# Kernel optimization log

Hardware: AMD Instinct MI355X
Metric: run time of the kernel (lower is better)

The kernel has to match this reference:

```python
import jax, jax.numpy as jnp
import numpy as np

D = 1024      # atrybuty (d_model)
H = 16        # kanaly (heads)
DH = D // H   # head dim
B, T = 4, 2048
EPS = 1e-5


def setup_inputs() -> dict:
    key = jax.random.key(0)
    ks = jax.random.split(key, 16)
    s = 0.02
    return {
        "x":  jax.random.normal(ks[0], (B, T, D), jnp.float32),
        "wq": jax.random.normal(ks[1], (D, D), jnp.float32) * s,
        "wk": jax.random.normal(ks[2], (D, D), jnp.float32) * s,
        "wv": jax.random.normal(ks[3], (D, D), jnp.float32) * s,
        "wp": jax.random.normal(ks[4], (D, D), jnp.float32) * s,
        "bp": jnp.zeros((D,), jnp.float32),
        "w1": jax.random.normal(ks[5], (D, 4 * D), jnp.float32) * s,
        "b1": jnp.zeros((4 * D,), jnp.float32),
        "w2": jax.random.normal(ks[6], (4 * D, D), jnp.float32) * s,
        "b2": jnp.zeros((D,), jnp.float32),
        "g1": jnp.ones((D,), jnp.float32),
        "be1": jnp.zeros((D,), jnp.float32),
        "g2": jnp.ones((D,), jnp.float32),
        "be2": jnp.zeros((D,), jnp.float32),
    }


def _layernorm(x, g, b):
    mu = jnp.mean(x, axis=-1, keepdims=True)
    var = jnp.mean(jnp.square(x - mu), axis=-1, keepdims=True)
    return (x - mu) * jax.lax.rsqrt(var + EPS) * g + b


def reference(x, wq, wk, wv, wp, bp, w1, b1, w2, b2, g1, be1, g2, be2):
    b, t, d = x.shape
    # --- self-attention on ln1(x) ---
    h = _layernorm(x, g1, be1)
    # per-head Linears are equivalent to one [D,D] projection split into heads
    q = (h @ wq).reshape(b, t, H, DH).transpose(0, 2, 1, 3)  # [B,H,T,Dh]
    k = (h @ wk).reshape(b, t, H, DH).transpose(0, 2, 1, 3)
    v = (h @ wv).reshape(b, t, H, DH).transpose(0, 2, 1, 3)
    # NOTE: original scales by full embed dim C, not head_dim
    scale = jnp.asarray(d, x.dtype) ** -0.5
    wei = jnp.einsum("bhqd,bhkd->bhqk", q, k) * scale
    causal = jnp.tril(jnp.ones((t, t), bool))
    wei = jnp.where(causal, wei, -jnp.inf)
    wei = jax.nn.softmax(wei, axis=-1)
    att = jnp.einsum("bhqk,bhkd->bhqd", wei, v)
    att = att.transpose(0, 2, 1, 3).reshape(b, t, d)
    x = x + att @ wp + bp
    # --- feedforward on ln2(x) ---
    h2 = _layernorm(x, g2, be2)
    x = x + jax.nn.relu(h2 @ w1 + b1) @ w2 + b2
    return x
```

## Files before the change

kernel.cpp:

```cpp
#include <hip/hip_runtime.h>
#include <hip/hip_bf16.h>
#include <stdint.h>

#define DM   1024
#define NH   16
#define DH   64
#define BATCH 4
#define SEQ  2048
#define MROWS (BATCH*SEQ)

typedef float f32x4 __attribute__((ext_vector_type(4)));
typedef __bf16 bf16x8 __attribute__((ext_vector_type(8)));
typedef short s16x4 __attribute__((ext_vector_type(4)));
typedef int   i32x2 __attribute__((ext_vector_type(2)));

#define QSCALE 0.045084220f

#define VM(n) asm volatile("s_waitcnt vmcnt(" #n ")" ::: "memory")
#define LGKM0 do { asm volatile("s_waitcnt lgkmcnt(0)" ::: "memory"); \
                   __builtin_amdgcn_sched_barrier(0); } while (0)

__device__ __forceinline__ short f2bs(float f) {
    __bf16 h = (__bf16)f;
    return __builtin_bit_cast(short, h);
}

__device__ __forceinline__ void gload_lds16(const void* g, void* l) {
    __builtin_amdgcn_global_load_lds(
        (__attribute__((address_space(1))) void*)(g),
        (__attribute__((address_space(3))) void*)(l), 16, 0, 0);
}

__device__ __forceinline__ void swz_xy(int ny, int& x, int& y) {
    const int bid = blockIdx.x;
    const int cpx = gridDim.x >> 3;
    const int wg  = (bid & 7) * cpx + (bid >> 3);
    x = wg / ny;
    y = wg % ny;
}

__global__ __launch_bounds__(256) void transpose_cvt_kernel(
    const float* __restrict__ w, short* __restrict__ wt, int K, int N)
{
    __shared__ short tile[64 * 65];
    const int k0 = blockIdx.x * 64, n0 = blockIdx.y * 64;
    const int t = threadIdx.x;
#pragma unroll
    for (int i = 0; i < 16; ++i) {
        int idx = i * 256 + t;
        int r = idx >> 6, c = idx & 63;
        tile[r * 65 + c] = f2bs(w[(size_t)(k0 + r) * N + n0 + c]);
    }
    __syncthreads();
#pragma unroll
    for (int i = 0; i < 16; ++i) {
        int idx = i * 256 + t;
        int r = idx >> 6, c = idx & 63;
        wt[(size_t)(n0 + r) * K + k0 + c] = tile[c * 65 + r];
    }
}

__global__ __launch_bounds__(256) void ln_kernel(
    const float* __restrict__ x, const float* __restrict__ g,
    const float* __restrict__ be, short* __restrict__ out)
{
    const int row = blockIdx.x, t = threadIdx.x;
    const float4 v = ((const float4*)(x + (size_t)row * DM))[t];
    float s  = v.x + v.y + v.z + v.w;
    float ss = v.x * v.x + v.y * v.y + v.z * v.z + v.w * v.w;
#pragma unroll
    for (int d = 1; d < 64; d <<= 1) {
        s  += __shfl_xor(s, d, 64);
        ss += __shfl_xor(ss, d, 64);
    }
    __shared__ float red[8];
    const int wid = t >> 6;
    if ((t & 63) == 0) { red[wid] = s; red[wid + 4] = ss; }
    __syncthreads();
    s  = red[0] + red[1] + red[2] + red[3];
    ss = red[4] + red[5] + red[6] + red[7];
    const float mu = s * (1.0f / DM);
    const float rs = rsqrtf(ss * (1.0f / DM) - mu * mu + 1e-5f);
    const float4 gg = ((const float4*)g)[t];
    const float4 bb = ((const float4*)be)[t];
    short4 o;
    o.x = f2bs((v.x - mu) * rs * gg.x + bb.x);
    o.y = f2bs((v.y - mu) * rs * gg.y + bb.y);
    o.z = f2bs((v.z - mu) * rs * gg.z + bb.z);
    o.w = f2bs((v.w - mu) * rs * gg.w + bb.w);
    ((short4*)(out + (size_t)row * DM))[t] = o;
}

template<int NCHUNK>
__device__ __forceinline__ void stage32(
    const short* __restrict__ G, int ldk, int row0, int k0,
    short* __restrict__ lds, int t)
{
#pragma unroll
    for (int i = 0; i < NCHUNK / 512; ++i) {
        const int c  = i * 512 + t;
        const int r  = c >> 2;
        const int sl = (c & 3) ^ ((r >> 1) & 3);
        gload_lds16(&G[(size_t)(row0 + r) * ldk + k0 + sl * 8], &lds[c * 8]);
    }
}

template<int EPI>
__global__ __launch_bounds__(512) void gemm256(
    const short* __restrict__ A, const short* __restrict__ Bt,
    int N, int K, int nyT,
    const float* __restrict__ bias, short* __restrict__ outb,
    short* __restrict__ qo, short* __restrict__ ko, short* __restrict__ vo)
{
    __shared__ short As[4][8192];
    __shared__ short Bs[4][8192];
    const int t = threadIdx.x, lane = t & 63, w = t >> 6;
    const int l15 = lane & 15, hi = lane >> 4;
    const int wm = (w >> 2) * 128, wn = (w & 3) * 64;
    int bx, by; swz_xy(nyT, bx, by);
    const int m0 = bx * 256, n0 = by * 256;
    const int NT = K >> 5;

    f32x4 acc[8][4] = {};

    stage32<1024>(A, K, m0, 0,  As[0], t); stage32<1024>(Bt, K, n0, 0,  Bs[0], t);
    stage32<1024>(A, K, m0, 32, As[1], t); stage32<1024>(Bt, K, n0, 32, Bs[1], t);
    stage32<1024>(A, K, m0, 64, As[2], t); stage32<1024>(Bt, K, n0, 64, Bs[2], t);
    VM(8);
    __builtin_amdgcn_s_barrier();

    for (int kt = 0; kt < NT; ++kt) {
        const short* Ac = As[kt & 3];
        const short* Bc = Bs[kt & 3];
        const int k3 = (kt + 3) << 5;
        bf16x8 af[8], bfr[4];

#pragma unroll
        for (int fm = 0; fm < 4; ++fm) {
            const int r = wm + fm * 16 + l15;
            af[fm] = *(const bf16x8*)&Ac[r * 32 + ((hi ^ ((r >> 1) & 3)) << 3)];
        }
#pragma unroll
        for (int fn = 0; fn < 4; ++fn) {
            const int r = wn + fn * 16 + l15;
            bfr[fn] = *(const bf16x8*)&Bc[r * 32 + ((hi ^ ((r >> 1) & 3)) << 3)];
        }
        if (kt + 3 < NT) stage32<1024>(A, K, m0, k3, As[(kt + 3) & 3], t);
        __builtin_amdgcn_s_barrier();
        LGKM0;
        __builtin_amdgcn_s_setprio(1);
#pragma unroll
        for (int fm = 0; fm < 4; ++fm)
#pragma unroll
            for (int fn = 0; fn < 4; ++fn)
                acc[fm][fn] = __builtin_amdgcn_mfma_f32_16x16x32_bf16(
                    af[fm], bfr[fn], acc[fm][fn], 0, 0, 0);
        __builtin_amdgcn_s_setprio(0);
        __builtin_amdgcn_s_barrier();

#pragma unroll
        for (int fm = 4; fm < 8; ++fm) {
            const int r = wm + fm * 16 + l15;
            af[fm] = *(const bf16x8*)&Ac[r * 32 + ((hi ^ ((r >> 1) & 3)) << 3)];
        }
        if (kt + 3 < NT) {
            stage32<1024>(Bt, K, n0, k3, Bs[(kt + 3) & 3], t);
            VM(8);
        } else if (kt + 2 < NT) VM(4);
        else if (kt + 1 < NT) VM(0);
        __builtin_amdgcn_s_barrier();
        LGKM0;
        __builtin_amdgcn_s_setprio(1);
#pragma unroll
        for (int fm = 4; fm < 8; ++fm)
#pragma unroll
            for (int fn = 0; fn < 4; ++fn)
                acc[fm][fn] = __builtin_amdgcn_mfma_f32_16x16x32_bf16(
                    af[fm], bfr[fn], acc[fm][fn], 0, 0, 0);
        __builtin_amdgcn_s_setprio(0);
        __builtin_amdgcn_s_barrier();
    }

#pragma unroll
    for (int fm = 0; fm < 8; ++fm)
#pragma unroll
        for (int fn = 0; fn < 4; ++fn) {
            const int row0 = m0 + wm + fm * 16 + hi * 4;
            const int nn = n0 + wn + fn * 16 + l15;
            const f32x4 a = acc[fm][fn];
            if constexpr (EPI == 0) {
                const int mat = nn >> 10, n1 = nn & 1023;
                const int head = n1 >> 6, dh = n1 & 63;
                if (mat == 2) {
                    const int tok = row0 & 2047, b = row0 >> 11;
                    const int tokp = (tok & ~63) |
                        (((((tok >> 3) & 7) ^ (dh & 7)) << 3)) | (tok & 7);
                    short4 pk;
                    pk.x = f2bs(a[0]); pk.y = f2bs(a[1]);
                    pk.z = f2bs(a[2]); pk.w = f2bs(a[3]);
                    *(short4*)&vo[((size_t)(b * NH + head) * DH + dh) * SEQ + tokp] = pk;
                } else if (mat == 1) {
#pragma unroll
                    for (int rr = 0; rr < 4; ++rr) {
                        const int m = row0 + rr;
                        const int b = m >> 11, tok = m & 2047;
                        const int dhp = (((dh >> 3) ^ (tok & 7)) << 3) | (dh & 7);
                        ko[((size_t)(b * NH + head) * SEQ + tok) * DH + dhp] =
                            f2bs(a[rr]);
                    }
                } else {
#pragma unroll
                    for (int rr = 0; rr < 4; ++rr) {
                        const int m = row0 + rr;
                        const int b = m >> 11, tok = m & 2047;
                        qo[((size_t)(b * NH + head) * SEQ + tok) * DH + dh] =
                            f2bs(a[rr] * QSCALE);
                    }
                }
            } else {
                const float bb = bias[nn];
#pragma unroll
                for (int rr = 0; rr < 4; ++rr) {
                    const float z = a[rr] + bb;
                    outb[(size_t)(row0 + rr) * N + nn] = f2bs(z > 0.f ? z : 0.f);
                }
            }
        }
}

__global__ __launch_bounds__(256) void gemm_bt128(
    const short* __restrict__ A, const short* __restrict__ Bt,
    int N, int K, int nyT,
    const float* __restrict__ bias, const float* __restrict__ res,
    float* __restrict__ outf)
{
    __shared__ short As[2][8192];
    __shared__ short Bs[2][8192];
    const int t = threadIdx.x, lane = t & 63, w = t >> 6;
    const int l15 = lane & 15, hi = lane >> 4;
    const int wm = (w & 1) * 64, wn = (w >> 1) * 64;
    int bx, by; swz_xy(nyT, bx, by);
    const int m0 = bx * 128, n0 = by * 128;
    const int NT = K >> 6;

    f32x4 acc[4][4] = {};

#define STAGE64(G, row0, k0, lds)                                             \
    do {                                                                      \
        _Pragma("unroll")                                                     \
        for (int i2 = 0; i2 < 4; ++i2) {                                      \
            const int c  = i2 * 256 + t;                                      \
            const int r  = c >> 3;                                            \
            const int sl = (c & 7) ^ (r & 7);                                 \
            gload_lds16(&(G)[(size_t)((row0) + r) * K + (k0) + sl * 8],       \
                        &(lds)[c * 8]);                                       \
        }                                                                     \
    } while (0)

    STAGE64(A, m0, 0, As[0]);
    STAGE64(Bt, n0, 0, Bs[0]);

    for (int kt = 0; kt < NT; ++kt) {
        if (kt + 1 < NT) {
            STAGE64(A,  m0, (kt + 1) << 6, As[(kt + 1) & 1]);
            STAGE64(Bt, n0, (kt + 1) << 6, Bs[(kt + 1) & 1]);
            VM(8);
        } else {
            VM(0);
        }
        __builtin_amdgcn_s_barrier();

        const short* Ac = As[kt & 1];
        const short* Bc = Bs[kt & 1];
        bf16x8 af[4][2], bfr[4][2];
#pragma unroll
        for (int fm = 0; fm < 4; ++fm) {
            const int r = wm + fm * 16 + l15;
#pragma unroll
            for (int ks = 0; ks < 2; ++ks)
                af[fm][ks] = *(const bf16x8*)
                    &Ac[r * 64 + (((ks * 4 + hi) ^ (r & 7)) << 3)];
        }
#pragma unroll
        for (int fn = 0; fn < 4; ++fn) {
            const int r = wn + fn * 16 + l15;
#pragma unroll
            for (int ks = 0; ks < 2; ++ks)
                bfr[fn][ks] = *(const bf16x8*)
                    &Bc[r * 64 + (((ks * 4 + hi) ^ (r & 7)) << 3)];
        }
#pragma unroll
        for (int ks = 0; ks < 2; ++ks)
#pragma unroll
            for (int fm = 0; fm < 4; ++fm)
#pragma unroll
                for (int fn = 0; fn < 4; ++fn)
                    acc[fm][fn] = __builtin_amdgcn_mfma_f32_16x16x32_bf16(
                        af[fm][ks], bfr[fn][ks], acc[fm][fn], 0, 0, 0);

        __builtin_amdgcn_s_barrier();
    }
#undef STAGE64

#pragma unroll
    for (int fm = 0; fm < 4; ++fm)
#pragma unroll
        for (int fn = 0; fn < 4; ++fn) {
            const int row0 = m0 + wm + fm * 16 + hi * 4;
            const int nn = n0 + wn + fn * 16 + l15;
            const float bb = bias[nn];
            const f32x4 a = acc[fm][fn];
#pragma unroll
            for (int rr = 0; rr < 4; ++rr) {
                const int m = row0 + rr;
                outf[(size_t)m * N + nn] = a[rr] + bb + res[(size_t)m * N + nn];
            }
        }
}

__global__ __launch_bounds__(512) void attn_kernel(
    const short* __restrict__ Q, const short* __restrict__ Kx,
    const short* __restrict__ Vt, short* __restrict__ att)
{
    __shared__ short Ks[2][2][4096];
    __shared__ short Vs[2][2][4096];

    const int n  = blockIdx.x;
    const int bh = n & 63;
    const int p  = n >> 6;
    const int tid = threadIdx.x;
    const int lane = tid & 63;
    const int wq = tid >> 6;
    const int l15 = lane & 15, hi = lane >> 4;
    const int qw = (wq < 4) ? (p * 128 + wq * 32)
                            : ((15 - p) * 128 + (wq - 4) * 32);
    const size_t base  = (size_t)bh * (SEQ * DH);
    const size_t vbase = (size_t)bh * (DH * SEQ);
    const int b = bh >> 4, head = bh & 15;

    bf16x8 qf[2][2];
#pragma unroll
    for (int mf = 0; mf < 2; ++mf)
#pragma unroll
        for (int kf = 0; kf < 2; ++kf)
            qf[mf][kf] = *(const bf16x8*)
                &Q[base + (size_t)(qw + mf * 16 + l15) * DH + kf * 32 + hi * 8];

    f32x4 O[2][4] = {};
    float L[2] = {0.f, 0.f};

    const int ndt    = 16 - p;
    const int nkv_wv = (qw + 95) >> 6;

#define STAGE_KV2(DT, BUF)                                                     \
    do {                                                                       \
        const int kvo = (DT) * 128;                                            \
        const int rw = tid >> 3, sl = tid & 7;                                 \
        _Pragma("unroll")                                                      \
        for (int sb = 0; sb < 2; ++sb) {                                       \
            gload_lds16(&Kx[base + (size_t)(kvo + sb * 64 + rw) * DH + sl * 8],\
                        &Ks[BUF][sb][tid * 8]);                                \
            gload_lds16(&Vt[vbase + (size_t)rw * SEQ + kvo + sb * 64 + sl * 8],\
                        &Vs[BUF][sb][tid * 8]);                                \
        }                                                                      \
    } while (0)

    STAGE_KV2(0, 0);

    for (int dt = 0; dt < ndt; ++dt) {
        VM(0);
        __builtin_amdgcn_s_barrier();
        if (dt + 1 < ndt) STAGE_KV2(dt + 1, (dt + 1) & 1);

#pragma unroll
        for (int sb = 0; sb < 2; ++sb) {
            const int t2 = dt * 2 + sb;
            if (t2 >= nkv_wv) break;
            const short* Kc = &Ks[dt & 1][sb][0];
            const short* Vc = &Vs[dt & 1][sb][0];
            const int kv0 = t2 * 64;

            bf16x8 kfr[4][2];
#pragma unroll
            for (int nf = 0; nf < 4; ++nf)
#pragma unroll
                for (int kf = 0; kf < 2; ++kf)
                    kfr[nf][kf] = *(const bf16x8*)
                        &Kc[(nf * 16 + l15) * 64 + (((kf * 4 + hi) ^ (l15 & 7)) << 3)];

            f32x4 St[4][2] = {};
#pragma unroll
            for (int kf = 0; kf < 2; ++kf)
#pragma unroll
                for (int nf = 0; nf < 4; ++nf)
#pragma unroll
                    for (int mf = 0; mf < 2; ++mf)
                        St[nf][mf] = __builtin_amdgcn_mfma_f32_16x16x32_bf16(
                            kfr[nf][kf], qf[mf][kf], St[nf][mf], 0, 0, 0);

            if (kv0 + 63 > qw) {
#pragma unroll
                for (int mf = 0; mf < 2; ++mf) {
                    const int q = qw + mf * 16 + l15;
#pragma unroll
                    for (int nf = 0; nf < 4; ++nf)
#pragma unroll
                        for (int r = 0; r < 4; ++r) {
                            const int kv = kv0 + nf * 16 + hi * 4 + r;
                            if (kv > q) St[nf][mf][r] = -3.0e38f;
                        }
                }
            }

            float lp[2] = {0.f, 0.f};
            s16x4 pa[4][2];
#pragma unroll
            for (int nf = 0; nf < 4; ++nf)
#pragma unroll
                for (int mf = 0; mf < 2; ++mf) {
                    const float p0 = exp2f(St[nf][mf][0]);
                    const float p1 = exp2f(St[nf][mf][1]);
                    const float p2 = exp2f(St[nf][mf][2]);
                    const float p3 = exp2f(St[nf][mf][3]);
                    lp[mf] += (p0 + p1) + (p2 + p3);
                    unsigned dw0, dw1;
                    asm("v_cvt_pk_bf16_f32 %0, %1, %2" : "=v"(dw0) : "v"(p0), "v"(p1));
                    asm("v_cvt_pk_bf16_f32 %0, %1, %2" : "=v"(dw1) : "v"(p2), "v"(p3));
                    i32x2 dd; dd[0] = (int)dw0; dd[1] = (int)dw1;
                    pa[nf][mf] = __builtin_bit_cast(s16x4, dd);
                }
            L[0] += lp[0]; L[1] += lp[1];

#pragma unroll
            for (int nf = 0; nf < 4; ++nf)
#pragma unroll
                for (int jf = 0; jf < 4; ++jf) {
                    const s16x4 vfr = *(const s16x4*)
                        &Vc[(jf * 16 + l15) * 64 +
                            ((((nf * 2 + (hi >> 1)) ^ (l15 & 7)) << 3) + ((hi & 1) << 2))];
#pragma unroll
                    for (int mf = 0; mf < 2; ++mf)
                        O[mf][jf] = __builtin_amdgcn_mfma_f32_16x16x16bf16_1k(
                            pa[nf][mf], vfr, O[mf][jf], 0, 0, 0);
                }
        }
    }
#undef STAGE_KV2

#pragma unroll
    for (int mf = 0; mf < 2; ++mf) {
        L[mf] += __shfl_xor(L[mf], 16, 64);
        L[mf] += __shfl_xor(L[mf], 32, 64);
    }
    const float inv0 = 1.0f / L[0], inv1 = 1.0f / L[1];

#pragma unroll
    for (int mf = 0; mf < 2; ++mf) {
        const float invm = mf ? inv1 : inv0;
#pragma unroll
        for (int r = 0; r < 4; ++r) {
            const int addr = ((lane >> 4) << 4) + (r << 2);
            const float iv = __builtin_bit_cast(float,
                __builtin_amdgcn_ds_bpermute(addr, __builtin_bit_cast(int, invm)));
            const int q = qw + mf * 16 + hi * 4 + r;
#pragma unroll
            for (int jf = 0; jf < 4; ++jf)
                att[(size_t)(b * SEQ + q) * DM + head * DH + jf * 16 + l15] =
                    f2bs(O[mf][jf][r] * iv);
        }
    }
}

extern "C" void kernel_launch(void* const* d_in, const int* in_sizes, int n_in,
                              void* d_out, int out_size, void* d_ws, size_t ws_size,
                              hipStream_t stream) {
    const float* x   = (const float*)d_in[0];
    const float* wq  = (const float*)d_in[1];
    const float* wk  = (const float*)d_in[2];
    const float* wv  = (const float*)d_in[3];
    const float* wp  = (const float*)d_in[4];
    const float* bp  = (const float*)d_in[5];
    const float* w1  = (const float*)d_in[6];
    const float* b1  = (const float*)d_in[7];
    const float* w2  = (const float*)d_in[8];
    const float* b2  = (const float*)d_in[9];
    const float* g1  = (const float*)d_in[10];
    const float* be1 = (const float*)d_in[11];
    const float* g2  = (const float*)d_in[12];
    const float* be2 = (const float*)d_in[13];
    float* out = (float*)d_out;

    char* ws = (char*)d_ws;
    short* wqkv_t = (short*)(ws + 0);
    short* wp_t   = (short*)(ws + 6291456);
    short* w1_t   = (short*)(ws + 8388608);
    short* w2_t   = (short*)(ws + 16777216);
    short* h      = (short*)(ws + 25165824);
    short* qb     = (short*)(ws + 41943040);
    short* kb     = (short*)(ws + 58720256);
    short* vb     = (short*)(ws + 75497472);
    short* att    = (short*)(ws + 92274688);
    float* x1     = (float*)(ws + 109051904);
    short* h2     = (short*)(ws + 142606336);
    short* tbuf   = (short*)(ws + 25165824);

    dim3 blk(256);

    transpose_cvt_kernel<<<dim3(16, 16), blk, 0, stream>>>(wq, wqkv_t,                1024, 1024);
    transpose_cvt_kernel<<<dim3(16, 16), blk, 0, stream>>>(wk, wqkv_t + 1024 * 1024,  1024, 1024);
    transpose_cvt_kernel<<<dim3(16, 16), blk, 0, stream>>>(wv, wqkv_t + 2048 * 1024,  1024, 1024);
    transpose_cvt_kernel<<<dim3(16, 16), blk, 0, stream>>>(wp, wp_t,                  1024, 1024);
    transpose_cvt_kernel<<<dim3(16, 64), blk, 0, stream>>>(w1, w1_t,                  1024, 4096);
    transpose_cvt_kernel<<<dim3(64, 16), blk, 0, stream>>>(w2, w2_t,                  4096, 1024);

    ln_kernel<<<MROWS, blk, 0, stream>>>(x, g1, be1, h);

    gemm256<0><<<dim3(384), dim3(512), 0, stream>>>(h, wqkv_t, 3072, 1024, 12,
        nullptr, nullptr, qb, kb, vb);

    attn_kernel<<<dim3(512), dim3(512), 0, stream>>>(qb, kb, vb, att);

    gemm_bt128<<<dim3(512), blk, 0, stream>>>(att, wp_t, 1024, 1024, 8,
        bp, x, x1);

    ln_kernel<<<MROWS, blk, 0, stream>>>(x1, g2, be2, h2);

    gemm256<2><<<dim3(512), dim3(512), 0, stream>>>(h2, w1_t, 4096, 1024, 16,
        b1, tbuf, nullptr, nullptr, nullptr);

    gemm_bt128<<<dim3(512), blk, 0, stream>>>(tbuf, w2_t, 1024, 4096, 8,
        b2, x1, out);
}
```

Measured before the change: 364.6 us.

## Replace 256x256 GEMM with 256x128 tile, 256-thread, double-buffered kernel

Replaces the 512-thread 256x256-tile GEMM, which used a 4-stage LDS pipeline with split half-tile MFMA phases and setprio, with a 256-thread kernel on 256x128 tiles and a simple 2-stage double buffer. The QKV and FFN1 launches double their grid to match the smaller N tile. The aim is more blocks per CU and less LDS per block, giving better occupancy and wave balance. In exchange, each block reuses its loaded data less, the prefetch distance shrinks from three stages to one, and the priority and phase-split scheduling is removed.

```diff
diff --git a/kernel.cpp b/kernel.cpp
--- a/kernel.cpp
+++ b/kernel.cpp
@@ -17,8 +17,6 @@
 #define QSCALE 0.045084220f
 
 #define VM(n) asm volatile("s_waitcnt vmcnt(" #n ")" ::: "memory")
-#define LGKM0 do { asm volatile("s_waitcnt lgkmcnt(0)" ::: "memory"); \
-                   __builtin_amdgcn_sched_barrier(0); } while (0)
 
 __device__ __forceinline__ short f2bs(float f) {
     __bf16 h = (__bf16)f;
@@ -91,52 +89,60 @@
     ((short4*)(out + (size_t)row * DM))[t] = o;
 }
 
-template<int NCHUNK>
-__device__ __forceinline__ void stage32(
-    const short* __restrict__ G, int ldk, int row0, int k0,
-    short* __restrict__ lds, int t)
-{
-#pragma unroll
-    for (int i = 0; i < NCHUNK / 512; ++i) {
-        const int c  = i * 512 + t;
-        const int r  = c >> 2;
-        const int sl = (c & 3) ^ ((r >> 1) & 3);
-        gload_lds16(&G[(size_t)(row0 + r) * ldk + k0 + sl * 8], &lds[c * 8]);
-    }
-}
-
 template<int EPI>
-__global__ __launch_bounds__(512) void gemm256(
+__global__ __launch_bounds__(256) void gemm128w(
     const short* __restrict__ A, const short* __restrict__ Bt,
     int N, int K, int nyT,
     const float* __restrict__ bias, short* __restrict__ outb,
     short* __restrict__ qo, short* __restrict__ ko, short* __restrict__ vo)
 {
-    __shared__ short As[4][8192];
-    __shared__ short Bs[4][8192];
+    __shared__ short As[2][8192];
+    __shared__ short Bs[2][4096];
     const int t = threadIdx.x, lane = t & 63, w = t >> 6;
     const int l15 = lane & 15, hi = lane >> 4;
-    const int wm = (w >> 2) * 128, wn = (w & 3) * 64;
+    const int wm = (w >> 1) * 128, wn = (w & 1) * 64;
     int bx, by; swz_xy(nyT, bx, by);
-    const int m0 = bx * 256, n0 = by * 256;
+    const int m0 = bx * 256, n0 = by * 128;
     const int NT = K >> 5;
 
     f32x4 acc[8][4] = {};
 
-    stage32<1024>(A, K, m0, 0,  As[0], t); stage32<1024>(Bt, K, n0, 0,  Bs[0], t);
-    stage32<1024>(A, K, m0, 32, As[1], t); stage32<1024>(Bt, K, n0, 32, Bs[1], t);
-    stage32<1024>(A, K, m0, 64, As[2], t); stage32<1024>(Bt, K, n0, 64, Bs[2], t);
-    VM(8);
-    __builtin_amdgcn_s_barrier();
+#define STAGEQ(k0, buf)                                                       \
+    do {                                                                      \
+        _Pragma("unroll")                                                     \
+        for (int i2 = 0; i2 < 4; ++i2) {                                      \
+            const int c  = i2 * 256 + t;                                      \
+            const int r  = c >> 2;                                            \
+            const int sl = (c & 3) ^ ((r >> 1) & 3);                          \
+            gload_lds16(&A[(size_t)(m0 + r) * K + (k0) + sl * 8],             \
+                        &As[buf][c * 8]);                                     \
+        }                                                                     \
+        _Pragma("unroll")                                                     \
+        for (int i2 = 0; i2 < 2; ++i2) {                                      \
+            const int c  = i2 * 256 + t;                                      \
+            const int r  = c >> 2;                                            \
+            const int sl = (c & 3) ^ ((r >> 1) & 3);                          \
+            gload_lds16(&Bt[(size_t)(n0 + r) * K + (k0) + sl * 8],            \
+                        &Bs[buf][c * 8]);                                     \
+        }                                                                     \
+    } while (0)
+
+    STAGEQ(0, 0);
 
     for (int kt = 0; kt < NT; ++kt) {
-        const short* Ac = As[kt & 3];
-        const short* Bc = Bs[kt & 3];
-        const int k3 = (kt + 3) << 5;
+        if (kt + 1 < NT) {
+            STAGEQ((kt + 1) << 5, (kt + 1) & 1);
+            VM(6);
+        } else {
+            VM(0);
+        }
+        __builtin_amdgcn_s_barrier();
+
+        const short* Ac = As[kt & 1];
+        const short* Bc = Bs[kt & 1];
         bf16x8 af[8], bfr[4];
-
-#pragma unroll
-        for (int fm = 0; fm < 4; ++fm) {
+#pragma unroll
+        for (int fm = 0; fm < 8; ++fm) {
             const int r = wm + fm * 16 + l15;
             af[fm] = *(const bf16x8*)&Ac[r * 32 + ((hi ^ ((r >> 1) & 3)) << 3)];
         }
@@ -145,41 +151,16 @@
             const int r = wn + fn * 16 + l15;
             bfr[fn] = *(const bf16x8*)&Bc[r * 32 + ((hi ^ ((r >> 1) & 3)) << 3)];
         }
-        if (kt + 3 < NT) stage32<1024>(A, K, m0, k3, As[(kt + 3) & 3], t);
-        __builtin_amdgcn_s_barrier();
-        LGKM0;
-        __builtin_amdgcn_s_setprio(1);
-#pragma unroll
-        for (int fm = 0; fm < 4; ++fm)
+#pragma unroll
+        for (int fm = 0; fm < 8; ++fm)
 #pragma unroll
             for (int fn = 0; fn < 4; ++fn)
                 acc[fm][fn] = __builtin_amdgcn_mfma_f32_16x16x32_bf16(
                     af[fm], bfr[fn], acc[fm][fn], 0, 0, 0);
-        __builtin_amdgcn_s_setprio(0);
+
         __builtin_amdgcn_s_barrier();
-
-#pragma unroll
-        for (int fm = 4; fm < 8; ++fm) {
-            const int r = wm + fm * 16 + l15;
-            af[fm] = *(const bf16x8*)&Ac[r * 32 + ((hi ^ ((r >> 1) & 3)) << 3)];
-        }
-        if (kt + 3 < NT) {
-            stage32<1024>(Bt, K, n0, k3, Bs[(kt + 3) & 3], t);
-            VM(8);
-        } else if (kt + 2 < NT) VM(4);
-        else if (kt + 1 < NT) VM(0);
-        __builtin_amdgcn_s_barrier();
-        LGKM0;
-        __builtin_amdgcn_s_setprio(1);
-#pragma unroll
-        for (int fm = 4; fm < 8; ++fm)
-#pragma unroll
-            for (int fn = 0; fn < 4; ++fn)
-                acc[fm][fn] = __builtin_amdgcn_mfma_f32_16x16x32_bf16(
-                    af[fm], bfr[fn], acc[fm][fn], 0, 0, 0);
-        __builtin_amdgcn_s_setprio(0);
-        __builtin_amdgcn_s_barrier();
-    }
+    }
+#undef STAGEQ
 
 #pragma unroll
     for (int fm = 0; fm < 8; ++fm)
@@ -515,7 +496,7 @@
 
     ln_kernel<<<MROWS, blk, 0, stream>>>(x, g1, be1, h);
 
-    gemm256<0><<<dim3(384), dim3(512), 0, stream>>>(h, wqkv_t, 3072, 1024, 12,
+    gemm128w<0><<<dim3(768), blk, 0, stream>>>(h, wqkv_t, 3072, 1024, 24,
         nullptr, nullptr, qb, kb, vb);
 
     attn_kernel<<<dim3(512), dim3(512), 0, stream>>>(qb, kb, vb, att);
@@ -525,7 +506,7 @@
 
     ln_kernel<<<MROWS, blk, 0, stream>>>(x1, g2, be2, h2);
 
-    gemm256<2><<<dim3(512), dim3(512), 0, stream>>>(h2, w1_t, 4096, 1024, 16,
+    gemm128w<2><<<dim3(1024), blk, 0, stream>>>(h2, w1_t, 4096, 1024, 32,
         b1, tbuf, nullptr, nullptr, nullptr);
 
     gemm_bt128<<<dim3(512), blk, 0, stream>>>(tbuf, w2_t, 1024, 4096, 8,
```

Result: slower. 453.6 us (+24.4%).
